# Optimization experiments

Hardware: AMD Instinct MI355X
Metric: run time of the kernel (lower is better)

Reference implementation:

```python
import jax, jax.numpy as jnp
import numpy as np

B, L, C, NEC = 1, 256, 1024, 2000


def setup_inputs() -> dict:
    key = jax.random.key(0)
    ks = jax.random.split(key, 8)
    attentions = jax.random.normal(ks[0], (B, L, C), jnp.float32)
    pooled = jax.random.normal(ks[1], (B, C), jnp.float32)
    attention_mask = jax.random.randint(ks[2], (B, L), 0, 2).astype(jnp.int32)
    lin1_w = jax.random.normal(ks[3], (C, C), jnp.float32) * 0.02
    lin1_b = jnp.zeros((C,), jnp.float32)
    cls_w = jax.random.normal(ks[4], (NEC, C), jnp.float32) * 0.02
    cls_b = jnp.zeros((NEC,), jnp.float32)
    conv1_w = jax.random.normal(ks[5], (C, 2 * C), jnp.float32) * 0.02  # 1x1 conv as matrix
    conv1_b = jnp.zeros((C,), jnp.float32)
    w2 = jax.random.normal(ks[6], (1, C, 7, 7), jnp.float32) * 0.02
    conv2_w = 0.5 * (w2 + jnp.swapaxes(w2, 2, 3))  # clip(): symmetrize kernel
    conv2_b = jnp.zeros((1,), jnp.float32)
    return dict(attentions=attentions, pooled=pooled, attention_mask=attention_mask,
                lin1_w=lin1_w, lin1_b=lin1_b, cls_w=cls_w, cls_b=cls_b,
                conv1_w=conv1_w, conv1_b=conv1_b, conv2_w=conv2_w, conv2_b=conv2_b)


def reference(attentions, pooled, attention_mask, lin1_w, lin1_b, cls_w, cls_b,
              conv1_w, conv1_b, conv2_w, conv2_b):
    # EC-classification head (dropout is identity at inference)
    logits = (pooled @ lin1_w.T + lin1_b) @ cls_w.T + cls_b  # [B, NEC]

    # mask out [CLS] (pos 0) and [SEP] (pos = sum of mask)
    s = attention_mask.sum(axis=1)
    mask = attention_mask.at[jnp.arange(B), s].set(0).at[:, 0].set(0)
    z = attentions * mask[:, :, None].astype(attentions.dtype)  # [B, L, C]
    z = jnp.swapaxes(z, 1, 2)                                   # [B, C, L]

    # pairwise |zi - zj| and zi * zj -> [B, 2C, L, L]
    z_diff = jnp.abs(z[:, :, None, :] - z[:, :, :, None])
    z_mul = z[:, :, None, :] * z[:, :, :, None]
    feat = jnp.concatenate([z_diff, z_mul], axis=1)

    # 1x1 conv (channel contraction) + ReLU
    h = jax.nn.relu(jnp.einsum('oc,bcij->boij', conv1_w, feat)
                    + conv1_b[None, :, None, None])            # [B, C, L, L]

    # 7x7 conv, padding 3, symmetric kernel, sigmoid
    out = jax.lax.conv_general_dilated(
        h, conv2_w, window_strides=(1, 1), padding=[(3, 3), (3, 3)],
        dimension_numbers=('NCHW', 'OIHW', 'NCHW')) + conv2_b[None, :, None, None]
    maps = jax.nn.sigmoid(out)                                  # [B, 1, L, L]
    return logits, maps.reshape(-1, L * L)
```

## Files before the change

kernel.cpp:

```cpp
#include <hip/hip_runtime.h>

typedef float  f4v    __attribute__((ext_vector_type(4)));
typedef __bf16 bf16x8 __attribute__((ext_vector_type(8)));
typedef __bf16 bf16x4 __attribute__((ext_vector_type(4)));

#define PCAP  16384
#define LDQ   16384
#define CH    1024
#define KI    2048
#define KIT   32

__device__ __forceinline__ int offA(int r, int A) { return r * A - ((r * (r - 1)) >> 1); }

__device__ __forceinline__ int mask_scan(const int* am, int t, int* act,
                                         unsigned long long* wm, int* wred) {
    int wave = t >> 6, lane = t & 63;
    int a = am[t];
    int sv = a;
#pragma unroll
    for (int d = 32; d; d >>= 1) sv += __shfl_down(sv, d);
    if (lane == 0) wred[wave] = sv;
    __syncthreads();
    int s = wred[0] + wred[1] + wred[2] + wred[3];
    int keep = (t != 0 && t != s && a != 0) ? 1 : 0;
    unsigned long long bm = __ballot(keep);
    if (lane == 0) wm[wave] = bm;
    __syncthreads();
    int base = 0, A = 0;
#pragma unroll
    for (int w = 0; w < 4; w++) {
        int pc = __popcll(wm[w]);
        if (w < wave) base += pc;
        A += pc;
    }
    if (keep) act[base + __popcll(bm & ((1ull << lane) - 1ull))] = t;
    __syncthreads();
    return A;
}

#define PB_FEATP  0
#define PB_FEATS  2048
#define PB_CVTA   2080
#define PB_K2     2592
#define PB_QCONST 2848
#define PB_ZERO   2897
#define PB_SCAN   3694
#define PB_HID    3695
#define PB_TOTAL  3951

__global__ void k_prep(const float* __restrict__ att, const int* __restrict__ am,
                       const float* __restrict__ c1w, const float* __restrict__ c2w,
                       const float* __restrict__ c1b,
                       const float* __restrict__ pooled, const float* __restrict__ lin1_w,
                       const float* __restrict__ lin1_b,
                       int* rank, int* counts, __bf16* featT, __bf16* A1p, __bf16* K2w,
                       float* Qc, float* Qzero, float* hid) {
    int b = blockIdx.x, t = threadIdx.x;

    if (b < PB_FEATS) {
        __shared__ int act[256];
        __shared__ unsigned long long wm[4];
        __shared__ int wred[4];
        int A = mask_scan(am, t, act, wm, wred);
        int P = (A * (A + 1)) >> 1;
        int Ppad = ((P + 127) >> 7) << 7;
        if (Ppad > PCAP) { Ppad = PCAP; P = PCAP; }
        int n0 = b * 8;
        if (n0 >= Ppad) return;
        int c0 = t * 4;
        float fA = (float)(2 * A + 1);
        for (int q = 0; q < 8; q++) {
            int n = n0 + q;
            bf16x8 ov;
            if (n < P && A > 0) {
                float disc = fmaxf(fA * fA - 8.0f * (float)n, 0.0f);
                int r = (int)floorf((fA - sqrtf(disc)) * 0.5f);
                r = min(A - 1, max(0, r));
                while (r > 0 && offA(r, A) > n) --r;
                while (r < A - 1 && offA(r + 1, A) <= n) ++r;
                int i = act[r], j = act[r + (n - offA(r, A))];
                float4 a = *(const float4*)&att[i * CH + c0];
                float4 bj = *(const float4*)&att[j * CH + c0];
                ov[0] = (__bf16)fabsf(a.x - bj.x); ov[1] = (__bf16)(a.x * bj.x);
                ov[2] = (__bf16)fabsf(a.y - bj.y); ov[3] = (__bf16)(a.y * bj.y);
                ov[4] = (__bf16)fabsf(a.z - bj.z); ov[5] = (__bf16)(a.z * bj.z);
                ov[6] = (__bf16)fabsf(a.w - bj.w); ov[7] = (__bf16)(a.w * bj.w);
            } else {
#pragma unroll
                for (int r8 = 0; r8 < 8; r8++) ov[r8] = (__bf16)0.0f;
            }
            *(bf16x8*)&featT[(size_t)n * KI + t * 8] = ov;
        }
    } else if (b < PB_CVTA) {
        int r0 = (b - PB_FEATS) * 8;
        int c0 = t * 4;
        for (int q = 0; q < 8; q++) {
            int r = r0 + q;
            float4 a = *(const float4*)&att[r * CH + c0];
            bf16x8 ov;
            ov[0] = (__bf16)fabsf(a.x); ov[1] = (__bf16)0.f;
            ov[2] = (__bf16)fabsf(a.y); ov[3] = (__bf16)0.f;
            ov[4] = (__bf16)fabsf(a.z); ov[5] = (__bf16)0.f;
            ov[6] = (__bf16)fabsf(a.w); ov[7] = (__bf16)0.f;
            *(bf16x8*)&featT[(size_t)(PCAP + r) * KI + t * 8] = ov;
        }
    } else if (b < PB_K2) {
        int gid = (b - PB_CVTA) * 256 + t;
        int o = gid >> 7, cw = (gid & 127) * 8;
        const float* wd = &c1w[o * 2048 + cw];
        const float* wmu = &c1w[o * 2048 + 1024 + cw];
        float4 d0 = *(const float4*)wd,  d1 = *(const float4*)(wd + 4);
        float4 m0 = *(const float4*)wmu, m1 = *(const float4*)(wmu + 4);
        bf16x8 v0, v1;
        v0[0] = (__bf16)d0.x; v0[1] = (__bf16)m0.x; v0[2] = (__bf16)d0.y; v0[3] = (__bf16)m0.y;
        v0[4] = (__bf16)d0.z; v0[5] = (__bf16)m0.z; v0[6] = (__bf16)d0.w; v0[7] = (__bf16)m0.w;
        v1[0] = (__bf16)d1.x; v1[1] = (__bf16)m1.x; v1[2] = (__bf16)d1.y; v1[3] = (__bf16)m1.y;
        v1[4] = (__bf16)d1.z; v1[5] = (__bf16)m1.z; v1[6] = (__bf16)d1.w; v1[7] = (__bf16)m1.w;
        *(bf16x8*)&A1p[o * 2048 + 2 * cw] = v0;
        *(bf16x8*)&A1p[o * 2048 + 2 * cw + 8] = v1;
    } else if (b < PB_QCONST) {
        int e = (b - PB_K2) * 256 + t;
        int trow = e >> 10, o = e & 1023;
        K2w[e] = (trow < 49) ? (__bf16)c2w[o * 49 + trow] : (__bf16)0.0f;
    } else if (b < PB_ZERO) {
        __shared__ float sh[256];
        int tap = b - PB_QCONST;
        float s = 0.f;
        for (int o = t; o < CH; o += 256) s += c2w[o * 49 + tap] * fmaxf(c1b[o], 0.f);
        sh[t] = s; __syncthreads();
        for (int d = 128; d; d >>= 1) { if (t < d) sh[t] += sh[t + d]; __syncthreads(); }
        if (t == 0) Qc[tap] = sh[0];
    } else if (b < PB_SCAN) {
        int idx = (b - PB_ZERO) * 256 + t;
        if (idx < 203840) {
            float4 zv = {0.f, 0.f, 0.f, 0.f};
            ((float4*)Qzero)[idx] = zv;
        }
    } else if (b == PB_SCAN) {
        __shared__ int act[256];
        __shared__ unsigned long long wm[4];
        __shared__ int wred[4];
        int A = mask_scan(am, t, act, wm, wred);
        int wave = t >> 6, lane = t & 63;
        int s = wred[0] + wred[1] + wred[2] + wred[3];
        int keep = (t != 0 && t != s && am[t] != 0) ? 1 : 0;
        int base = 0;
#pragma unroll
        for (int w = 0; w < 4; w++) if (w < wave) base += __popcll(wm[w]);
        unsigned long long bm = wm[wave];
        rank[t] = keep ? (base + __popcll(bm & ((1ull << lane) - 1ull))) : -1;
        if (t == 0) {
            int P = (A * (A + 1)) >> 1;
            int Pp = ((P + 127) >> 7) << 7;
            if (Pp > PCAP) Pp = PCAP;
            counts[0] = A; counts[1] = P; counts[2] = Pp;
        }
    } else {
        int o = (b - PB_HID) * 4 + (t >> 6);
        int lane = t & 63;
        const float* row = lin1_w + (size_t)o * CH;
        float s = 0.f;
        for (int c = lane; c < CH; c += 64) s += pooled[c] * row[c];
        for (int d = 32; d; d >>= 1) s += __shfl_down(s, d);
        if (lane == 0) hid[o] = s + lin1_b[o];
    }
}

__global__ __launch_bounds__(512) void gemm_fused(
        const __bf16* __restrict__ A1p, const __bf16* __restrict__ featT,
        const __bf16* __restrict__ K2w, const float* __restrict__ c1b,
        const int* __restrict__ counts,
        float* __restrict__ Q, float* __restrict__ Qs,
        const float* __restrict__ hid, const float* __restrict__ cls_w,
        const float* __restrict__ cls_b, float* __restrict__ logits) {
    int x = blockIdx.x, y = blockIdx.y;
    int tid = threadIdx.x, wave = tid >> 6, lane = tid & 63;

    if (x == 8) {
#pragma unroll
        for (int rr = 0; rr < 2; rr++) {
            int o = y * 16 + wave * 2 + rr;
            if (o >= 2000) break;
            const float* row = cls_w + (size_t)o * CH;
            float s = 0.f;
            for (int c = lane; c < CH; c += 64) s += hid[c] * row[c];
            for (int d = 32; d; d >>= 1) s += __shfl_down(s, d);
            if (lane == 0) logits[o] = s + cls_b[o];
        }
        return;
    }

    int Ppad = counts[2];
    int ntp = Ppad >> 7;
    int ntiles = ntp + 2;
    int c_rt = (ntiles + 7) >> 3;
    int g = (x + y) & 7;
    int nbl = y >> 3, mb = y & 7;
    if (nbl >= c_rt) return;
    int nb = g * c_rt + nbl;
    if (nb >= ntiles) return;
    bool sing = (nb >= ntp);
    int brow = sing ? (PCAP + (nb - ntp) * 128) : nb * 128;

    __shared__ __align__(16) char smemraw[65536];
#define ASP(bsel) ((__bf16(*)[64])(smemraw + (bsel) * 16384))
#define BSP(bsel) ((__bf16(*)[64])(smemraw + 32768 + (bsel) * 16384))
#define HTL ((__bf16(*)[136])(smemraw))
#define K2L ((__bf16(*)[136])(smemraw + 34816))

    int lanerow = lane >> 3;
    int swchunk = ((lane & 7) ^ lanerow) * 8;
    const __bf16* srcA = A1p + (size_t)(mb * 128 + wave * 16 + lanerow) * KI + swchunk;
    const __bf16* srcB = featT + (size_t)(brow + wave * 16 + lanerow) * KI + swchunk;

    f4v acc[4][2] = {};
    int row16 = lane & 15, quad = lane >> 4;
    int wx = wave & 3, wy = wave >> 2;

#define STAGE(kt, bsel)                                                           \
    {                                                                             \
        const __bf16* sA = srcA + (kt) * 64;                                      \
        _Pragma("unroll")                                                         \
        for (int q = 0; q < 2; q++) {                                             \
            __builtin_amdgcn_global_load_lds(                                     \
                (const __attribute__((address_space(1))) void*)(sA + (size_t)q * 8 * KI), \
                (__attribute__((address_space(3))) void*)&ASP(bsel)[wave * 16 + q * 8][0], 16, 0, 0); \
        }                                                                         \
        const __bf16* sB = srcB + (kt) * 64;                                      \
        _Pragma("unroll")                                                         \
        for (int q = 0; q < 2; q++) {                                             \
            __builtin_amdgcn_global_load_lds(                                     \
                (const __attribute__((address_space(1))) void*)(sB + (size_t)q * 8 * KI), \
                (__attribute__((address_space(3))) void*)&BSP(bsel)[wave * 16 + q * 8][0], 16, 0, 0); \
        }                                                                         \
    }

    STAGE(0, 0);
    for (int kt = 0; kt < KIT; ++kt) {
        int cur = kt & 1;
        if (kt + 1 < KIT) {
            STAGE(kt + 1, cur ^ 1);
            __builtin_amdgcn_s_waitcnt(0xF74);
        } else {
            __builtin_amdgcn_s_waitcnt(0xF70);
        }
        __builtin_amdgcn_s_barrier();
#pragma unroll
        for (int ks = 0; ks < 2; ks++) {
            bf16x8 a[4], b[2];
            int col = ((ks * 4 + quad) ^ (row16 & 7)) * 8;
#pragma unroll
            for (int mt = 0; mt < 4; mt++)
                a[mt] = *(const bf16x8*)&ASP(cur)[wy * 64 + mt * 16 + row16][col];
#pragma unroll
            for (int nt = 0; nt < 2; nt++)
                b[nt] = *(const bf16x8*)&BSP(cur)[wx * 32 + nt * 16 + row16][col];
#pragma unroll
            for (int mt = 0; mt < 4; mt++)
#pragma unroll
                for (int nt = 0; nt < 2; nt++)
                    acc[mt][nt] = __builtin_amdgcn_mfma_f32_16x16x32_bf16(a[mt], b[nt], acc[mt][nt], 0, 0, 0);
        }
        __builtin_amdgcn_s_barrier();
    }
#undef STAGE

#pragma unroll
    for (int it = 0; it < 2; it++) {
        int gid = it * 512 + tid;
        int trow = gid >> 4, oc = (gid & 15) * 8;
        bf16x8 kv = *(const bf16x8*)&K2w[(size_t)trow * CH + mb * 128 + oc];
        *(bf16x8*)&K2L[trow][oc] = kv;
    }
#pragma unroll
    for (int mt = 0; mt < 4; mt++) {
        int ol = wy * 64 + mt * 16 + quad * 4;
        float4 bv = *(const float4*)&c1b[mb * 128 + ol];
#pragma unroll
        for (int nt = 0; nt < 2; nt++) {
            int n = wx * 32 + nt * 16 + row16;
            bf16x4 pk;
            pk[0] = (__bf16)fmaxf(acc[mt][nt][0] + bv.x, 0.f);
            pk[1] = (__bf16)fmaxf(acc[mt][nt][1] + bv.y, 0.f);
            pk[2] = (__bf16)fmaxf(acc[mt][nt][2] + bv.z, 0.f);
            pk[3] = (__bf16)fmaxf(acc[mt][nt][3] + bv.w, 0.f);
            *(bf16x4*)&HTL[n][ol] = pk;
        }
    }
    __syncthreads();

    int tq = wave & 3, nhalf = wave >> 2;
    f4v acc2[4] = {};
#pragma unroll
    for (int ko = 0; ko < 4; ko++) {
        bf16x8 af = *(const bf16x8*)&K2L[tq * 16 + row16][ko * 32 + quad * 8];
#pragma unroll
        for (int nt = 0; nt < 4; nt++) {
            bf16x8 bf_ = *(const bf16x8*)&HTL[nhalf * 64 + nt * 16 + row16][ko * 32 + quad * 8];
            acc2[nt] = __builtin_amdgcn_mfma_f32_16x16x32_bf16(af, bf_, acc2[nt], 0, 0, 0);
        }
    }

    float* Qdst = sing ? Qs : Q;
    int ldq = sing ? 256 : LDQ;
    int nbase = sing ? (nb - ntp) * 128 : nb * 128;
    int t0 = tq * 16 + quad * 4;
#pragma unroll
    for (int nt = 0; nt < 4; nt++) {
        int n = nbase + nhalf * 64 + nt * 16 + row16;
#pragma unroll
        for (int r = 0; r < 4; r++)
            if (t0 + r < 49) atomicAdd(&Qdst[(size_t)(t0 + r) * ldq + n], acc2[nt][r]);
    }
#undef ASP
#undef BSP
#undef HTL
#undef K2L
}

__global__ __launch_bounds__(1024) void k_out(
                      const float* __restrict__ Q, const float* __restrict__ Qs,
                      const float* __restrict__ Qc, const int* __restrict__ rank,
                      const int* __restrict__ counts, const float* b2,
                      float* __restrict__ outmaps) {
    __shared__ int rankL[256];
    __shared__ float part[1024];
    int tt_ = threadIdx.x, i = blockIdx.x;
    int t = tt_ & 255;
    int quarter = tt_ >> 8;
    if (tt_ < 256) rankL[tt_] = rank[tt_];
    __syncthreads();
    int A = counts[0];
    int j = t;

    int qc_[7], rq_[7], oq_[7];
    bool vq_[7];
#pragma unroll
    for (int dj = 0; dj < 7; dj++) {
        int q = j + dj - 3;
        vq_[dj] = ((unsigned)q <= 255u);
        int qc = min(255, max(0, q));
        qc_[dj] = qc;
        int r = rankL[qc];
        rq_[dj] = r;
        oq_[dj] = offA(max(r, 0), A);
    }

    float acc = (quarter == 0) ? b2[0] : 0.f;
#pragma unroll
    for (int di = 0; di < 7; di++) {
        int p = i + di - 3;
        bool vp = ((unsigned)p <= 255u);
        int pc = min(255, max(0, p));
        int rp = rankL[pc];
        int op = offA(max(rp, 0), A);
#pragma unroll
        for (int dj = 0; dj < 7; dj++) {
            int tt = di * 7 + dj;
            if ((tt & 3) != quarter) continue;
            int qc = qc_[dj];
            bool pfirst = (pc <= qc);
            int a  = pfirst ? pc : qc;
            int bb = pfirst ? qc : pc;
            int ra = pfirst ? rp : rq_[dj];
            int rb = pfirst ? rq_[dj] : rp;
            int oa = pfirst ? op : oq_[dj];
            const float* s1 = (rb >= 0) ? (Q + (size_t)tt * LDQ + (oa + rb - ra))
                                        : (Qs + tt * 256 + a);
            const float* s0 = (rb >= 0) ? (Qs + tt * 256 + bb)
                                        : (Qc + tt);
            const float* sp = (ra >= 0) ? s1 : s0;
            float val = *sp;
            acc = (vp && vq_[dj]) ? (acc + val) : acc;
        }
    }
    part[tt_] = acc;
    __syncthreads();
    if (tt_ < 256) {
        float s = (part[tt_] + part[tt_ + 256]) + (part[tt_ + 512] + part[tt_ + 768]);
        outmaps[i * 256 + j] = 1.0f / (1.0f + expf(-s));
    }
}


extern "C" void kernel_launch(void* const* d_in, const int* in_sizes, int n_in,
                              void* d_out, int out_size, void* d_ws, size_t ws_size,
                              hipStream_t stream) {
    const float* att    = (const float*)d_in[0];
    const float* pooled = (const float*)d_in[1];
    const int*   am     = (const int*)d_in[2];
    const float* lin1_w = (const float*)d_in[3];
    const float* lin1_b = (const float*)d_in[4];
    const float* cls_w  = (const float*)d_in[5];
    const float* cls_b  = (const float*)d_in[6];
    const float* c1w    = (const float*)d_in[7];
    const float* c1b    = (const float*)d_in[8];
    const float* c2w    = (const float*)d_in[9];
    const float* c2b    = (const float*)d_in[10];
    float* out = (float*)d_out;
    char*  ws  = (char*)d_ws;

    __bf16* A1p  = (__bf16*)(ws);
    __bf16* K2w  = (__bf16*)(ws + 4194304);
    float*  Q    = (float*) (ws + 4325376);
    float*  Qs   = (float*) (ws + 7536640);
    float*  Qc   = (float*) (ws + 7586816);
    int*    rank = (int*)   (ws + 7587072);
    float*  hid  = (float*) (ws + 7588096);
    int*    counts=(int*)   (ws + 7592192);
    __bf16* featT= (__bf16*)(ws + 7592960);

    k_prep<<<PB_TOTAL, 256, 0, stream>>>(att, am, c1w, c2w, c1b, pooled, lin1_w, lin1_b,
                                         rank, counts, featT, A1p, K2w, Qc, Q, hid);

    gemm_fused<<<dim3(9, 136), 512, 0, stream>>>(A1p, featT, K2w, c1b, counts, Q, Qs,
                                                 hid, cls_w, cls_b, out);

    k_out<<<256, 1024, 0, stream>>>(Q, Qs, Qc, rank, counts, c2b, out + 2000);
}
```

Baseline: 147.3 us.

## Build pairwise feature tiles on the fly inside the GEMM instead of materializing featT

Stops writing the packed pairwise feature matrix (|zi-zj|, zi*zj in bf16) to global memory in the prep kernel. The GEMM instead decodes the (i,j) pair for each of its 128 columns and loads the fp32 attention rows, then computes and packs the bf16 features straight into LDS. This removes a large global write and re-read of featT. In exchange the GEMM does more ALU work, uses register-staged loads in place of async global-to-LDS copies for B, syncs with full barriers, and adds a launch-bounds occupancy hint.

```diff
diff --git a/kernel.cpp b/kernel.cpp
--- a/kernel.cpp
+++ b/kernel.cpp
@@ -38,74 +38,25 @@
     return A;
 }
 
-#define PB_FEATP  0
-#define PB_FEATS  2048
-#define PB_CVTA   2080
-#define PB_K2     2592
-#define PB_QCONST 2848
-#define PB_ZERO   2897
-#define PB_SCAN   3694
-#define PB_HID    3695
-#define PB_TOTAL  3951
+#define PB_CVTA   0
+#define PB_K2     512
+#define PB_QCONST 768
+#define PB_ZERO   817
+#define PB_SCAN   1614
+#define PB_HID    1615
+#define PB_TOTAL  1871
 
 __global__ void k_prep(const float* __restrict__ att, const int* __restrict__ am,
                        const float* __restrict__ c1w, const float* __restrict__ c2w,
                        const float* __restrict__ c1b,
                        const float* __restrict__ pooled, const float* __restrict__ lin1_w,
                        const float* __restrict__ lin1_b,
-                       int* rank, int* counts, __bf16* featT, __bf16* A1p, __bf16* K2w,
+                       int* rank, int* counts, int* actg, __bf16* A1p, __bf16* K2w,
                        float* Qc, float* Qzero, float* hid) {
     int b = blockIdx.x, t = threadIdx.x;
 
-    if (b < PB_FEATS) {
-        __shared__ int act[256];
-        __shared__ unsigned long long wm[4];
-        __shared__ int wred[4];
-        int A = mask_scan(am, t, act, wm, wred);
-        int P = (A * (A + 1)) >> 1;
-        int Ppad = ((P + 127) >> 7) << 7;
-        if (Ppad > PCAP) { Ppad = PCAP; P = PCAP; }
-        int n0 = b * 8;
-        if (n0 >= Ppad) return;
-        int c0 = t * 4;
-        float fA = (float)(2 * A + 1);
-        for (int q = 0; q < 8; q++) {
-            int n = n0 + q;
-            bf16x8 ov;
-            if (n < P && A > 0) {
-                float disc = fmaxf(fA * fA - 8.0f * (float)n, 0.0f);
-                int r = (int)floorf((fA - sqrtf(disc)) * 0.5f);
-                r = min(A - 1, max(0, r));
-                while (r > 0 && offA(r, A) > n) --r;
-                while (r < A - 1 && offA(r + 1, A) <= n) ++r;
-                int i = act[r], j = act[r + (n - offA(r, A))];
-                float4 a = *(const float4*)&att[i * CH + c0];
-                float4 bj = *(const float4*)&att[j * CH + c0];
-                ov[0] = (__bf16)fabsf(a.x - bj.x); ov[1] = (__bf16)(a.x * bj.x);
-                ov[2] = (__bf16)fabsf(a.y - bj.y); ov[3] = (__bf16)(a.y * bj.y);
-                ov[4] = (__bf16)fabsf(a.z - bj.z); ov[5] = (__bf16)(a.z * bj.z);
-                ov[6] = (__bf16)fabsf(a.w - bj.w); ov[7] = (__bf16)(a.w * bj.w);
-            } else {
-#pragma unroll
-                for (int r8 = 0; r8 < 8; r8++) ov[r8] = (__bf16)0.0f;
-            }
-            *(bf16x8*)&featT[(size_t)n * KI + t * 8] = ov;
-        }
-    } else if (b < PB_CVTA) {
-        int r0 = (b - PB_FEATS) * 8;
-        int c0 = t * 4;
-        for (int q = 0; q < 8; q++) {
-            int r = r0 + q;
-            float4 a = *(const float4*)&att[r * CH + c0];
-            bf16x8 ov;
-            ov[0] = (__bf16)fabsf(a.x); ov[1] = (__bf16)0.f;
-            ov[2] = (__bf16)fabsf(a.y); ov[3] = (__bf16)0.f;
-            ov[4] = (__bf16)fabsf(a.z); ov[5] = (__bf16)0.f;
-            ov[6] = (__bf16)fabsf(a.w); ov[7] = (__bf16)0.f;
-            *(bf16x8*)&featT[(size_t)(PCAP + r) * KI + t * 8] = ov;
-        }
-    } else if (b < PB_K2) {
-        int gid = (b - PB_CVTA) * 256 + t;
+    if (b < PB_K2) {
+        int gid = b * 256 + t;
         int o = gid >> 7, cw = (gid & 127) * 8;
         const float* wd = &c1w[o * 2048 + cw];
         const float* wmu = &c1w[o * 2048 + 1024 + cw];
@@ -149,6 +100,7 @@
         for (int w = 0; w < 4; w++) if (w < wave) base += __popcll(wm[w]);
         unsigned long long bm = wm[wave];
         rank[t] = keep ? (base + __popcll(bm & ((1ull << lane) - 1ull))) : -1;
+        actg[t] = (t < A) ? act[t] : 0;
         if (t == 0) {
             int P = (A * (A + 1)) >> 1;
             int Pp = ((P + 127) >> 7) << 7;
@@ -166,8 +118,9 @@
     }
 }
 
-__global__ __launch_bounds__(512) void gemm_fused(
-        const __bf16* __restrict__ A1p, const __bf16* __restrict__ featT,
+__global__ __launch_bounds__(512, 4) void gemm_fused(
+        const __bf16* __restrict__ A1p, const float* __restrict__ att,
+        const int* __restrict__ actg,
         const __bf16* __restrict__ K2w, const float* __restrict__ c1b,
         const int* __restrict__ counts,
         float* __restrict__ Q, float* __restrict__ Qs,
@@ -190,6 +143,8 @@
         return;
     }
 
+    int A = counts[0];
+    int P = counts[1]; if (P > PCAP) P = PCAP;
     int Ppad = counts[2];
     int ntp = Ppad >> 7;
     int ntiles = ntp + 2;
@@ -200,24 +155,55 @@
     int nb = g * c_rt + nbl;
     if (nb >= ntiles) return;
     bool sing = (nb >= ntp);
-    int brow = sing ? (PCAP + (nb - ntp) * 128) : nb * 128;
 
     __shared__ __align__(16) char smemraw[65536];
+    __shared__ int pairs[256];
 #define ASP(bsel) ((__bf16(*)[64])(smemraw + (bsel) * 16384))
 #define BSP(bsel) ((__bf16(*)[64])(smemraw + 32768 + (bsel) * 16384))
 #define HTL ((__bf16(*)[136])(smemraw))
 #define K2L ((__bf16(*)[136])(smemraw + 34816))
 
+    if (tid < 128) {
+        int i = -1, j = -1;
+        if (sing) {
+            i = (nb - ntp) * 128 + tid;
+            j = -2;
+        } else {
+            int n = nb * 128 + tid;
+            if (n < P && A > 0) {
+                float fA = (float)(2 * A + 1);
+                float disc = fmaxf(fA * fA - 8.0f * (float)n, 0.0f);
+                int r = (int)floorf((fA - sqrtf(disc)) * 0.5f);
+                r = min(A - 1, max(0, r));
+                while (r > 0 && offA(r, A) > n) --r;
+                while (r < A - 1 && offA(r + 1, A) <= n) ++r;
+                i = actg[r]; j = actg[r + (n - offA(r, A))];
+            }
+        }
+        pairs[2 * tid] = i; pairs[2 * tid + 1] = j;
+    }
+
     int lanerow = lane >> 3;
     int swchunk = ((lane & 7) ^ lanerow) * 8;
     const __bf16* srcA = A1p + (size_t)(mb * 128 + wave * 16 + lanerow) * KI + swchunk;
-    const __bf16* srcB = featT + (size_t)(brow + wave * 16 + lanerow) * KI + swchunk;
+
+    __syncthreads();
+
+    int myrow = tid >> 2, q4 = tid & 3;
+    int pi = pairs[2 * myrow], pj = pairs[2 * myrow + 1];
+    const float* attI = att + (size_t)max(pi, 0) * CH;
+    const float* attJ = att + (size_t)max(pj, 0) * CH;
+    bool vi = pi >= 0, vj = pj >= 0;
+    int sw0 = ((2 * q4) ^ (myrow & 7)) * 8;
+    int sw1 = ((2 * q4 + 1) ^ (myrow & 7)) * 8;
 
     f4v acc[4][2] = {};
     int row16 = lane & 15, quad = lane >> 4;
     int wx = wave & 3, wy = wave >> 2;
-
-#define STAGE(kt, bsel)                                                           \
+    float4 zero4 = {0.f, 0.f, 0.f, 0.f};
+    float4 pA0, pA1, pB0, pB1;
+
+#define STAGEA(kt, bsel)                                                          \
     {                                                                             \
         const __bf16* sA = srcA + (kt) * 64;                                      \
         _Pragma("unroll")                                                         \
@@ -226,25 +212,43 @@
                 (const __attribute__((address_space(1))) void*)(sA + (size_t)q * 8 * KI), \
                 (__attribute__((address_space(3))) void*)&ASP(bsel)[wave * 16 + q * 8][0], 16, 0, 0); \
         }                                                                         \
-        const __bf16* sB = srcB + (kt) * 64;                                      \
-        _Pragma("unroll")                                                         \
-        for (int q = 0; q < 2; q++) {                                             \
-            __builtin_amdgcn_global_load_lds(                                     \
-                (const __attribute__((address_space(1))) void*)(sB + (size_t)q * 8 * KI), \
-                (__attribute__((address_space(3))) void*)&BSP(bsel)[wave * 16 + q * 8][0], 16, 0, 0); \
-        }                                                                         \
-    }
-
-    STAGE(0, 0);
+    }
+
+#define LOADATT(kt)                                                               \
+    {                                                                             \
+        int cb = (kt) * 32 + q4 * 8;                                              \
+        pA0 = vi ? *(const float4*)&attI[cb]     : zero4;                         \
+        pA1 = vi ? *(const float4*)&attI[cb + 4] : zero4;                         \
+        pB0 = vj ? *(const float4*)&attJ[cb]     : zero4;                         \
+        pB1 = vj ? *(const float4*)&attJ[cb + 4] : zero4;                         \
+    }
+
+#define PACKB(bsel)                                                               \
+    {                                                                             \
+        bf16x8 v0, v1;                                                            \
+        v0[0] = (__bf16)fabsf(pA0.x - pB0.x); v0[1] = (__bf16)(pA0.x * pB0.x);    \
+        v0[2] = (__bf16)fabsf(pA0.y - pB0.y); v0[3] = (__bf16)(pA0.y * pB0.y);    \
+        v0[4] = (__bf16)fabsf(pA0.z - pB0.z); v0[5] = (__bf16)(pA0.z * pB0.z);    \
+        v0[6] = (__bf16)fabsf(pA0.w - pB0.w); v0[7] = (__bf16)(pA0.w * pB0.w);    \
+        v1[0] = (__bf16)fabsf(pA1.x - pB1.x); v1[1] = (__bf16)(pA1.x * pB1.x);    \
+        v1[2] = (__bf16)fabsf(pA1.y - pB1.y); v1[3] = (__bf16)(pA1.y * pB1.y);    \
+        v1[4] = (__bf16)fabsf(pA1.z - pB1.z); v1[5] = (__bf16)(pA1.z * pB1.z);    \
+        v1[6] = (__bf16)fabsf(pA1.w - pB1.w); v1[7] = (__bf16)(pA1.w * pB1.w);    \
+        *(bf16x8*)&BSP(bsel)[myrow][sw0] = v0;                                    \
+        *(bf16x8*)&BSP(bsel)[myrow][sw1] = v1;                                    \
+    }
+
+    LOADATT(0);
+    STAGEA(0, 0);
+    PACKB(0);
+    __syncthreads();
+
     for (int kt = 0; kt < KIT; ++kt) {
         int cur = kt & 1;
         if (kt + 1 < KIT) {
-            STAGE(kt + 1, cur ^ 1);
-            __builtin_amdgcn_s_waitcnt(0xF74);
-        } else {
-            __builtin_amdgcn_s_waitcnt(0xF70);
-        }
-        __builtin_amdgcn_s_barrier();
+            LOADATT(kt + 1);
+            STAGEA(kt + 1, cur ^ 1);
+        }
 #pragma unroll
         for (int ks = 0; ks < 2; ks++) {
             bf16x8 a[4], b[2];
@@ -261,9 +265,12 @@
                 for (int nt = 0; nt < 2; nt++)
                     acc[mt][nt] = __builtin_amdgcn_mfma_f32_16x16x32_bf16(a[mt], b[nt], acc[mt][nt], 0, 0, 0);
         }
-        __builtin_amdgcn_s_barrier();
-    }
-#undef STAGE
+        if (kt + 1 < KIT) PACKB(cur ^ 1);
+        __syncthreads();
+    }
+#undef STAGEA
+#undef LOADATT
+#undef PACKB
 
 #pragma unroll
     for (int it = 0; it < 2; it++) {
@@ -408,12 +415,12 @@
     int*    rank = (int*)   (ws + 7587072);
     float*  hid  = (float*) (ws + 7588096);
     int*    counts=(int*)   (ws + 7592192);
-    __bf16* featT= (__bf16*)(ws + 7592960);
+    int*    actg = (int*)   (ws + 7592960);
 
     k_prep<<<PB_TOTAL, 256, 0, stream>>>(att, am, c1w, c2w, c1b, pooled, lin1_w, lin1_b,
-                                         rank, counts, featT, A1p, K2w, Qc, Q, hid);
-
-    gemm_fused<<<dim3(9, 136), 512, 0, stream>>>(A1p, featT, K2w, c1b, counts, Q, Qs,
+                                         rank, counts, actg, A1p, K2w, Qc, Q, hid);
+
+    gemm_fused<<<dim3(9, 136), 512, 0, stream>>>(A1p, att, actg, K2w, c1b, counts, Q, Qs,
                                                  hid, cls_w, cls_b, out);
 
     k_out<<<256, 1024, 0, stream>>>(Q, Qs, Qc, rank, counts, c2b, out + 2000);
```

New measurement: 261.6 us. +77.6%, slower.
